# Optimization experiments

Hardware: AMD Instinct MI355X
Metric: run time of the kernel (lower is better)

## Reference

```python
import jax, jax.numpy as jnp
import numpy as np

HID, NH_FULL, K, GAMMA = 768, 12, 9, 2
HD = HID // NH_FULL            # 64
NH = NH_FULL // GAMMA          # 6
RH = HD * NH                   # 384 reduced hidden dim
OUT_HALF = HID // 2            # 384
B, S = 8, 1024


def setup_inputs() -> dict:
    key0 = jax.random.key(0)
    ks = jax.random.split(key0, 20)
    r = lambda i, shape, sc=0.02: (jax.random.normal(ks[i], shape, dtype=jnp.float32) * sc)
    inp = {
        'query': jax.random.normal(ks[0], (B, S, HID), dtype=jnp.float32),
        'mask': jnp.ones((B, 1, 1, S), dtype=jnp.int32),
        # q/k/v projections: hidden -> reduced
        'Wq': r(1, (HID, RH)), 'bq': jnp.zeros((RH,), jnp.float32),
        'Wk': r(2, (HID, RH)), 'bk': jnp.zeros((RH,), jnp.float32),
        'Wv': r(3, (HID, RH)), 'bv': jnp.zeros((RH,), jnp.float32),
        # depthwise separable conv: depthwise [HID,1,K] + pointwise [RH,HID]
        'dw_w': r(4, (HID, 1, K), 0.1), 'dw_b': jnp.zeros((HID,), jnp.float32),
        'pw_w': r(5, (RH, HID)), 'pw_b': jnp.zeros((RH,), jnp.float32),
        # self-attn output proj: reduced -> hidden//2
        'Wsa': r(6, (RH, OUT_HALF)), 'bsa': jnp.zeros((OUT_HALF,), jnp.float32),
        # dynamic kernel layer: reduced -> K*NH
        'Wdk': r(7, (RH, K * NH)), 'bdk': jnp.zeros((K * NH,), jnp.float32),
        # dynamic attn output proj: reduced -> hidden//2
        'Wda': r(8, (RH, OUT_HALF)), 'bda': jnp.zeros((OUT_HALF,), jnp.float32),
    }
    # self_attn=True requires query==key==value
    inp['key'] = inp['query']
    inp['value'] = inp['query']
    return inp


def _forward(query, key, value, mask, Wq, bq, Wk, bk, Wv, bv,
             dw_w, dw_b, pw_w, pw_b, Wsa, bsa, Wdk, bdk, Wda, bda):
    b, s, _ = query.shape
    q = query @ Wq + bq          # [B,S,RH]
    k = key @ Wk + bk
    v = value @ Wv + bv

    # ---- depthwise separable conv over key (seq axis), 'same' padding ----
    key_t = jnp.transpose(key, (0, 2, 1))  # [B,HID,S]
    dw = jax.lax.conv_general_dilated(
        key_t, dw_w, window_strides=(1,), padding=[(K // 2, K // 2)],
        feature_group_count=HID, dimension_numbers=('NCH', 'OIH', 'NCH'))
    dw = dw + dw_b[None, :, None]          # [B,HID,S]
    ks_feat = jnp.einsum('bhs,rh->bsr', dw, pw_w) + pw_b  # [B,S,RH]

    # ---- standard multi-head self-attention branch ----
    def split(x):  # [B,S,RH] -> [B,NH,S,HD]
        return x.reshape(b, s, NH, HD).transpose(0, 2, 1, 3)
    qh, kh, vh = split(q), split(k), split(v)
    scores = jnp.einsum('bhqd,bhkd->bhqk', qh, kh) / jnp.sqrt(jnp.float32(HD))
    scores = jnp.where(mask == 0, jnp.float32(-jnp.inf), scores)
    attn_wts = jax.nn.softmax(scores, axis=-1)             # [B,NH,S,S]
    attn_out = jnp.einsum('bhqk,bhkd->bhqd', attn_wts, vh)
    attn_out = attn_out.transpose(0, 2, 1, 3).reshape(b, s, RH)
    self_out = attn_out @ Wsa + bsa                         # [B,S,HID//2]

    # ---- span dynamic conv attention branch ----
    # unfold v into sliding windows: expanded[b,s,h,d,k] = v_pad[b, s+k, h*HD+d]
    v_pad = jnp.pad(v, ((0, 0), (K // 2, K // 2), (0, 0)))  # [B,S+K-1,RH]
    windows = jnp.stack([v_pad[:, i:i + s] for i in range(K)], axis=-1)  # [B,S,RH,K]
    windows = windows.reshape(b, s, NH, HD, K)
    dyn_logits = (q * ks_feat) @ Wdk + bdk                  # [B,S,K*NH]
    dyn_kernel = jax.nn.softmax(dyn_logits.reshape(b, s, NH, K), axis=-1)
    dyn_out = jnp.einsum('bshdk,bshk->bshd', windows, dyn_kernel).reshape(b, s, RH)
    dyn_out = dyn_out @ Wda + bda                           # [B,S,HID//2]

    return attn_wts, jnp.concatenate([self_out, dyn_out], axis=-1)


def reference(query, key, value, mask, Wq, bq, Wk, bk, Wv, bv,
              dw_w, dw_b, pw_w, pw_b, Wsa, bsa, Wdk, bdk, Wda, bda):
    return _forward(query, key, value, mask, Wq, bq, Wk, bk, Wv, bv,
                    dw_w, dw_b, pw_w, pw_b, Wsa, bsa, Wdk, bdk, Wda, bda)
```

## Files before the change

kernel.cpp:

```cpp
#include <hip/hip_runtime.h>
#include <math.h>

#define B 8
#define S 1024
#define HID 768
#define RH 384
#define NH 6
#define HD 64
#define KW 9
#define KNH 54
#define OUTHALF 384
#define QLD 1152
#define EXPSCALE 0.18033688f

typedef __attribute__((ext_vector_type(8))) short short8;
typedef __attribute__((ext_vector_type(4))) float f32x4;

#define SWZ(r, c) (((r) << 6) + ((c) ^ (((r) & 7) << 3)))

__device__ __forceinline__ ushort f2bf(float x) {
    unsigned u = __float_as_uint(x);
    u += 0x7FFF + ((u >> 16) & 1);
    return (ushort)(u >> 16);
}
__device__ __forceinline__ float bf2f(ushort u) {
    return __uint_as_float(((unsigned)u) << 16);
}
__device__ __forceinline__ short8 cvt8(const float* p) {
    short8 r;
    #pragma unroll
    for (int i = 0; i < 8; i++) r[i] = (short)f2bf(p[i]);
    return r;
}

__global__ __launch_bounds__(256) void cvt_dw_fused(
    const float* __restrict__ query, const float* __restrict__ dw_w,
    const float* __restrict__ dw_b, ushort* __restrict__ Xbf,
    ushort* __restrict__ dwout)
{
    int idx = blockIdx.x*256 + threadIdx.x;
    if (idx >= B*S*(HID/8)) return;
    int c0 = (idx % (HID/8))*8;
    int s  = (idx / (HID/8)) % S;
    int b  = idx / ((HID/8)*S);

    float ctr[8];
    *(float4*)&ctr[0] = *(const float4*)(query + ((size_t)b*S + s)*HID + c0);
    *(float4*)&ctr[4] = *(const float4*)(query + ((size_t)b*S + s)*HID + c0 + 4);
    *(short8*)(Xbf + ((size_t)b*S + s)*HID + c0) = cvt8(ctr);

    float acc[8];
    *(float4*)&acc[0] = *(const float4*)(dw_b + c0);
    *(float4*)&acc[4] = *(const float4*)(dw_b + c0 + 4);
    #pragma unroll
    for (int kk = 0; kk < KW; kk++) {
        int sp = s + kk - KW/2;
        if (sp >= 0 && sp < S) {
            float row[8];
            *(float4*)&row[0] = *(const float4*)(query + ((size_t)b*S + sp)*HID + c0);
            *(float4*)&row[4] = *(const float4*)(query + ((size_t)b*S + sp)*HID + c0 + 4);
            #pragma unroll
            for (int j = 0; j < 8; j++)
                acc[j] += row[j] * dw_w[(c0+j)*KW + kk];
        }
    }
    *(short8*)(dwout + ((size_t)b*S + s)*HID + c0) = cvt8(acc);
}

__global__ __launch_bounds__(256) void prep_weights(
    const float* __restrict__ Wq, const float* __restrict__ Wk, const float* __restrict__ Wv,
    const float* __restrict__ bq, const float* __restrict__ bk, const float* __restrict__ bv,
    const float* __restrict__ pw_w, const float* __restrict__ Wsa,
    const float* __restrict__ Wda, const float* __restrict__ Wdk,
    ushort* __restrict__ WqkvT, ushort* __restrict__ pw_bf,
    ushort* __restrict__ WsaT, ushort* __restrict__ WdaT, ushort* __restrict__ WdkT,
    float* __restrict__ bqkv)
{
    int i = blockIdx.x*256 + threadIdx.x;
    if (i < 884736) {
        int n = i / 768, kk = i % 768;
        int w = n / 384, nn = n % 384;
        const float* W = (w == 0) ? Wq : (w == 1) ? Wk : Wv;
        WqkvT[i] = f2bf(W[kk*384 + nn]);
        return;
    }
    i -= 884736;
    if (i < 294912) { pw_bf[i] = f2bf(pw_w[i]); return; }
    i -= 294912;
    if (i < 147456) {
        int n = i / 384, kk = i % 384;
        WsaT[i] = f2bf(Wsa[kk*384 + n]);
        return;
    }
    i -= 147456;
    if (i < 147456) {
        int n = i / 384, kk = i % 384;
        WdaT[i] = f2bf(Wda[kk*384 + n]);
        return;
    }
    i -= 147456;
    if (i < 49152) {
        int n = i / 384, kk = i % 384;
        WdkT[i] = (n < KNH) ? f2bf(Wdk[kk*KNH + n]) : (ushort)0;
        return;
    }
    i -= 49152;
    if (i < 1152) {
        bqkv[i] = (i < 384) ? bq[i] : (i < 768) ? bk[i-384] : bv[i-768];
    }
}

template<bool OUTBF>
__global__ __launch_bounds__(256) void gemm_mfma(
    const ushort* __restrict__ A, const ushort* __restrict__ Bt,
    const float* __restrict__ bias, void* __restrict__ Cout,
    int N, int Kd, int ldc)
{
    __shared__ __attribute__((aligned(16))) ushort As[128*32];
    __shared__ __attribute__((aligned(16))) ushort Bs[128*32];
    const int t = threadIdx.x;
    const int wave = t >> 6, lane = t & 63;
    const int lr = lane & 15, lg = lane >> 4;
    const int wr = wave >> 1, wc = wave & 1;
    const int bm = blockIdx.y * 128, bn = blockIdx.x * 128;

    f32x4 acc[4][4] = {};
    const int srow = t >> 1, sseg = t & 1;
    const ushort* Arow = A + (size_t)(bm + srow)*Kd + sseg*16;
    const ushort* Brow = Bt + (size_t)(bn + srow)*Kd + sseg*16;
    const int g0 = (sseg*2) ^ (srow & 3), g1 = (sseg*2 + 1) ^ (srow & 3);
    const int swz = lg ^ (lr & 3);

    for (int k0 = 0; k0 < Kd; k0 += 32) {
        short8 av0 = *(const short8*)(Arow + k0);
        short8 av1 = *(const short8*)(Arow + k0 + 8);
        short8 bv0 = *(const short8*)(Brow + k0);
        short8 bv1 = *(const short8*)(Brow + k0 + 8);
        __syncthreads();
        *(short8*)&As[srow*32 + g0*8] = av0;
        *(short8*)&As[srow*32 + g1*8] = av1;
        *(short8*)&Bs[srow*32 + g0*8] = bv0;
        *(short8*)&Bs[srow*32 + g1*8] = bv1;
        __syncthreads();
        short8 af[4], bfr[4];
        #pragma unroll
        for (int m = 0; m < 4; m++)
            af[m] = *(const short8*)&As[(wr*64 + m*16 + lr)*32 + swz*8];
        #pragma unroll
        for (int n = 0; n < 4; n++)
            bfr[n] = *(const short8*)&Bs[(wc*64 + n*16 + lr)*32 + swz*8];
        #pragma unroll
        for (int m = 0; m < 4; m++)
            #pragma unroll
            for (int n = 0; n < 4; n++)
                acc[m][n] = __builtin_amdgcn_mfma_f32_16x16x32_bf16(af[m], bfr[n], acc[m][n], 0, 0, 0);
    }

    #pragma unroll
    for (int m = 0; m < 4; m++) {
        #pragma unroll
        for (int n = 0; n < 4; n++) {
            int gcol = bn + wc*64 + n*16 + lr;
            if (gcol >= N) continue;
            float bz = bias[gcol];
            #pragma unroll
            for (int r = 0; r < 4; r++) {
                size_t grow = bm + wr*64 + m*16 + lg*4 + r;
                float val = acc[m][n][r] + bz;
                if (OUTBF) ((ushort*)Cout)[grow*ldc + gcol] = f2bf(val);
                else       ((float*)Cout)[grow*ldc + gcol] = val;
            }
        }
    }
}

template<bool OUTBF, bool DUAL>
__global__ __launch_bounds__(256) void gemm64(
    const ushort* __restrict__ A0, const ushort* __restrict__ Bt0,
    const float* __restrict__ bias0, void* __restrict__ C0,
    const ushort* __restrict__ A1, const ushort* __restrict__ Bt1,
    const float* __restrict__ bias1,
    int N, int Kd, int ldc)
{
    __shared__ __attribute__((aligned(16))) ushort As[64*32];
    __shared__ __attribute__((aligned(16))) ushort Bs[64*32];
    const ushort* A  = (DUAL && blockIdx.z) ? A1 : A0;
    const ushort* Bt = (DUAL && blockIdx.z) ? Bt1 : Bt0;
    const float* bias = (DUAL && blockIdx.z) ? bias1 : bias0;
    const int coff = (DUAL && blockIdx.z) ? OUTHALF : 0;

    const int t = threadIdx.x;
    const int wave = t >> 6, lane = t & 63;
    const int lr = lane & 15, lg = lane >> 4;
    const int wr = wave >> 1, wc = wave & 1;
    const int bm = blockIdx.y * 64, bn = blockIdx.x * 64;

    f32x4 acc[2][2] = {};
    const int srow = t >> 2, sseg = t & 3;
    const ushort* Arow = A + (size_t)(bm + srow)*Kd + sseg*8;
    const ushort* Brow = Bt + (size_t)(bn + srow)*Kd + sseg*8;
    const int gs = sseg ^ (srow & 3);
    const int swz = lg ^ (lr & 3);

    for (int k0 = 0; k0 < Kd; k0 += 32) {
        short8 av = *(const short8*)(Arow + k0);
        short8 bv = *(const short8*)(Brow + k0);
        __syncthreads();
        *(short8*)&As[srow*32 + gs*8] = av;
        *(short8*)&Bs[srow*32 + gs*8] = bv;
        __syncthreads();
        short8 af[2], bfr[2];
        #pragma unroll
        for (int m = 0; m < 2; m++)
            af[m] = *(const short8*)&As[(wr*32 + m*16 + lr)*32 + swz*8];
        #pragma unroll
        for (int n = 0; n < 2; n++)
            bfr[n] = *(const short8*)&Bs[(wc*32 + n*16 + lr)*32 + swz*8];
        #pragma unroll
        for (int m = 0; m < 2; m++)
            #pragma unroll
            for (int n = 0; n < 2; n++)
                acc[m][n] = __builtin_amdgcn_mfma_f32_16x16x32_bf16(af[m], bfr[n], acc[m][n], 0, 0, 0);
    }

    #pragma unroll
    for (int m = 0; m < 2; m++) {
        #pragma unroll
        for (int n = 0; n < 2; n++) {
            int gcol = bn + wc*32 + n*16 + lr;
            if (gcol >= N) continue;
            float bz = bias[gcol];
            #pragma unroll
            for (int r = 0; r < 4; r++) {
                size_t grow = bm + wr*32 + m*16 + lg*4 + r;
                float val = acc[m][n][r] + bz;
                if (OUTBF) ((ushort*)C0)[grow*ldc + gcol + coff] = f2bf(val);
                else       ((float*)C0)[grow*ldc + gcol + coff] = val;
            }
        }
    }
}

__global__ __launch_bounds__(64) void gemm_qksdk(
    const ushort* __restrict__ qkv, const float* __restrict__ ksf,
    const ushort* __restrict__ WdkT, const float* __restrict__ bdk,
    float* __restrict__ dynlog)
{
    const int lane = threadIdx.x;
    const int lr = lane & 15, lg = lane >> 4;
    const int r0 = blockIdx.x * 16;
    const int row = r0 + lr;

    f32x4 acc[4] = {};
    for (int ks = 0; ks < RH/32; ks++) {
        int k0 = ks*32 + lg*8;
        short8 qv = *(const short8*)(qkv + (size_t)row*QLD + k0);
        float kf[8];
        *(float4*)&kf[0] = *(const float4*)(ksf + (size_t)row*RH + k0);
        *(float4*)&kf[4] = *(const float4*)(ksf + (size_t)row*RH + k0 + 4);
        short8 afr;
        #pragma unroll
        for (int j = 0; j < 8; j++)
            afr[j] = (short)f2bf(bf2f((ushort)qv[j]) * kf[j]);
        #pragma unroll
        for (int t4 = 0; t4 < 4; t4++) {
            short8 bfr = *(const short8*)(WdkT + (size_t)(t4*16 + lr)*RH + k0);
            acc[t4] = __builtin_amdgcn_mfma_f32_16x16x32_bf16(afr, bfr, acc[t4], 0, 0, 0);
        }
    }
    #pragma unroll
    for (int t4 = 0; t4 < 4; t4++) {
        int n = t4*16 + lr;
        if (n >= KNH) continue;
        float bz = bdk[n];
        #pragma unroll
        for (int r = 0; r < 4; r++)
            dynlog[(size_t)(r0 + lg*4 + r)*KNH + n] = acc[t4][r] + bz;
    }
}

__global__ __launch_bounds__(256) void attn_fused(
    const ushort* __restrict__ qkv, const int* __restrict__ mask,
    float* __restrict__ out0, ushort* __restrict__ attnws)
{
    __shared__ __attribute__((aligned(16))) ushort Ks[64*64];
    __shared__ __attribute__((aligned(16))) ushort Vt[64*64];
    __shared__ __attribute__((aligned(16))) ushort Ps[4][16*64];

    const int b = blockIdx.z, h = blockIdx.y, q0 = blockIdx.x * 64;
    const int t = threadIdx.x;
    const int wave = t >> 6, lane = t & 63;
    const int lr = lane & 15, lg = lane >> 4;

    const ushort* qrow = qkv + (size_t)(b*S + q0 + wave*16 + lr)*QLD + h*HD;
    short8 aQ0 = *(const short8*)(qrow + lg*8);
    short8 aQ1 = *(const short8*)(qrow + 32 + lg*8);

    const int srow = t >> 2;
    const int sseg = t & 3;
    const int* mrow = mask + b*S;
    const ushort* kbase = qkv + RH;
    const ushort* vbase = qkv + 2*RH;

    float lsum[4] = {0.f, 0.f, 0.f, 0.f};

    for (int kc = 0; kc < S; kc += 64) {
        const ushort* kr = kbase + (size_t)(b*S + kc + srow)*QLD + h*HD + sseg*16;
        short8 kv0 = *(const short8*)(kr);
        short8 kv1 = *(const short8*)(kr + 8);
        __syncthreads();
        *(short8*)&Ks[SWZ(srow, sseg*16)]     = kv0;
        *(short8*)&Ks[SWZ(srow, sseg*16 + 8)] = kv1;
        __syncthreads();
        #pragma unroll
        for (int t4 = 0; t4 < 4; t4++) {
            short8 b0 = *(const short8*)&Ks[SWZ(t4*16 + lr, lg*8)];
            short8 b1 = *(const short8*)&Ks[SWZ(t4*16 + lr, 32 + lg*8)];
            f32x4 c = {0.f, 0.f, 0.f, 0.f};
            c = __builtin_amdgcn_mfma_f32_16x16x32_bf16(aQ0, b0, c, 0, 0, 0);
            c = __builtin_amdgcn_mfma_f32_16x16x32_bf16(aQ1, b1, c, 0, 0, 0);
            float add = mrow[kc + t4*16 + lr] ? 0.f : -1e30f;
            #pragma unroll
            for (int r = 0; r < 4; r++)
                lsum[r] += exp2f(c[r]*EXPSCALE + add);
        }
    }
    #pragma unroll
    for (int r = 0; r < 4; r++) {
        #pragma unroll
        for (int off = 1; off < 16; off <<= 1)
            lsum[r] += __shfl_xor(lsum[r], off, 16);
    }
    float inv[4];
    #pragma unroll
    for (int r = 0; r < 4; r++) inv[r] = 1.f / lsum[r];

    f32x4 o[4] = {};
    ushort* Psw = &Ps[wave][0];
    const size_t obase = ((size_t)((b*NH + h)*S) + q0 + wave*16) * (size_t)S;

    for (int kc = 0; kc < S; kc += 64) {
        const ushort* kr = kbase + (size_t)(b*S + kc + srow)*QLD + h*HD + sseg*16;
        short8 kv0 = *(const short8*)(kr);
        short8 kv1 = *(const short8*)(kr + 8);
        ushort vb[16];
        #pragma unroll
        for (int i = 0; i < 16; i++)
            vb[i] = vbase[(size_t)(b*S + kc + sseg*16 + i)*QLD + h*HD + srow];
        __syncthreads();
        *(short8*)&Ks[SWZ(srow, sseg*16)]     = kv0;
        *(short8*)&Ks[SWZ(srow, sseg*16 + 8)] = kv1;
        *(short8*)&Vt[SWZ(srow, sseg*16)]     = *(short8*)&vb[0];
        *(short8*)&Vt[SWZ(srow, sseg*16 + 8)] = *(short8*)&vb[8];
        __syncthreads();

        #pragma unroll
        for (int t4 = 0; t4 < 4; t4++) {
            short8 b0 = *(const short8*)&Ks[SWZ(t4*16 + lr, lg*8)];
            short8 b1 = *(const short8*)&Ks[SWZ(t4*16 + lr, 32 + lg*8)];
            f32x4 c = {0.f, 0.f, 0.f, 0.f};
            c = __builtin_amdgcn_mfma_f32_16x16x32_bf16(aQ0, b0, c, 0, 0, 0);
            c = __builtin_amdgcn_mfma_f32_16x16x32_bf16(aQ1, b1, c, 0, 0, 0);
            float add = mrow[kc + t4*16 + lr] ? 0.f : -1e30f;
            #pragma unroll
            for (int r = 0; r < 4; r++) {
                float p = exp2f(c[r]*EXPSCALE + add) * inv[r];
                out0[obase + (size_t)(lg*4 + r)*S + kc + t4*16 + lr] = p;
                Psw[SWZ(lg*4 + r, t4*16 + lr)] = f2bf(p);
            }
        }
        #pragma unroll
        for (int kh = 0; kh < 2; kh++) {
            short8 pa = *(const short8*)&Psw[SWZ(lr, kh*32 + lg*8)];
            #pragma unroll
            for (int dt = 0; dt < 4; dt++) {
                short8 vv = *(const short8*)&Vt[SWZ(dt*16 + lr, kh*32 + lg*8)];
                o[dt] = __builtin_amdgcn_mfma_f32_16x16x32_bf16(pa, vv, o[dt], 0, 0, 0);
            }
        }
    }

    #pragma unroll
    for (int dt = 0; dt < 4; dt++)
        #pragma unroll
        for (int r = 0; r < 4; r++)
            attnws[(size_t)(b*S + q0 + wave*16 + lg*4 + r)*RH + h*HD + dt*16 + lr] = f2bf(o[dt][r]);
}

__global__ __launch_bounds__(256) void dyn_conv(
    const float* __restrict__ logits, const ushort* __restrict__ qkv,
    ushort* __restrict__ dynout)
{
    int idx = blockIdx.x*256 + threadIdx.x;
    if (idx >= B*S*(RH/4)) return;
    int r4 = (idx % (RH/4))*4;
    int s  = (idx / (RH/4)) % S;
    int b  = idx / ((RH/4)*S);
    int h  = r4 / HD;
    const float* lg = logits + ((size_t)b*S + s)*KNH + h*KW;
    float mx = lg[0];
    #pragma unroll
    for (int kk = 1; kk < KW; kk++) mx = fmaxf(mx, lg[kk]);
    float e[KW], sum = 0.f;
    #pragma unroll
    for (int kk = 0; kk < KW; kk++) { e[kk] = __expf(lg[kk]-mx); sum += e[kk]; }
    float inv = 1.f/sum;
    float acc[4] = {0.f, 0.f, 0.f, 0.f};
    const ushort* vbase = qkv + 2*RH;
    #pragma unroll
    for (int kk = 0; kk < KW; kk++) {
        int sp = s + kk - KW/2;
        if (sp >= 0 && sp < S) {
            const ushort* vp = vbase + (size_t)(b*S + sp)*QLD + r4;
            #pragma unroll
            for (int j = 0; j < 4; j++) acc[j] += bf2f(vp[j]) * e[kk];
        }
    }
    ushort4 o;
    o.x = f2bf(acc[0]*inv); o.y = f2bf(acc[1]*inv);
    o.z = f2bf(acc[2]*inv); o.w = f2bf(acc[3]*inv);
    *(ushort4*)(dynout + ((size_t)b*S + s)*RH + r4) = o;
}

extern "C" void kernel_launch(void* const* d_in, const int* in_sizes, int n_in,
                              void* d_out, int out_size, void* d_ws, size_t ws_size,
                              hipStream_t stream) {
    const float* query = (const float*)d_in[0];
    const int*   mask  = (const int*)d_in[1];
    const float* Wq    = (const float*)d_in[2];
    const float* bq    = (const float*)d_in[3];
    const float* Wk    = (const float*)d_in[4];
    const float* bk    = (const float*)d_in[5];
    const float* Wv    = (const float*)d_in[6];
    const float* bv    = (const float*)d_in[7];
    const float* dw_w  = (const float*)d_in[8];
    const float* dw_b  = (const float*)d_in[9];
    const float* pw_w  = (const float*)d_in[10];
    const float* pw_b  = (const float*)d_in[11];
    const float* Wsa   = (const float*)d_in[12];
    const float* bsa   = (const float*)d_in[13];
    const float* Wdk   = (const float*)d_in[14];
    const float* bdk   = (const float*)d_in[15];
    const float* Wda   = (const float*)d_in[16];
    const float* bda   = (const float*)d_in[17];

    float* out0 = (float*)d_out;
    float* out1 = out0 + (size_t)B*NH*S*S;

    char* wsb = (char*)d_ws;
    size_t off = 0;
    auto alloc = [&](size_t bytes) { char* p = wsb + off; off += (bytes + 255) & ~255ull; return p; };
    ushort* Xbf    = (ushort*)alloc((size_t)B*S*HID*2);
    ushort* qkvbf  = (ushort*)alloc((size_t)B*S*QLD*2);
    ushort* dwbf   = (ushort*)alloc((size_t)B*S*HID*2);
    float*  ksf    = (float*) alloc((size_t)B*S*RH*4);
    ushort* attnbf = (ushort*)alloc((size_t)B*S*RH*2);
    ushort* dynbf  = (ushort*)alloc((size_t)B*S*RH*2);
    float*  dynlog = (float*) alloc((size_t)B*S*KNH*4);
    ushort* WqkvT  = (ushort*)alloc((size_t)QLD*HID*2);
    ushort* pw_bf  = (ushort*)alloc((size_t)RH*HID*2);
    ushort* WsaT   = (ushort*)alloc((size_t)RH*RH*2);
    ushort* WdaT   = (ushort*)alloc((size_t)RH*RH*2);
    ushort* WdkT   = (ushort*)alloc((size_t)128*RH*2);
    float*  bqkv   = (float*) alloc((size_t)QLD*4);

    const int M = B*S;

    prep_weights<<<(1524864 + 255)/256, 256, 0, stream>>>(
        Wq, Wk, Wv, bq, bk, bv, pw_w, Wsa, Wda, Wdk,
        WqkvT, pw_bf, WsaT, WdaT, WdkT, bqkv);

    cvt_dw_fused<<<(M*(HID/8) + 255)/256, 256, 0, stream>>>(query, dw_w, dw_b, Xbf, dwbf);

    gemm_mfma<true><<<dim3(QLD/128, M/128), 256, 0, stream>>>(
        Xbf, WqkvT, bqkv, qkvbf, QLD, HID, QLD);

    gemm64<false, false><<<dim3(RH/64, M/64), 256, 0, stream>>>(
        dwbf, pw_bf, pw_b, ksf, nullptr, nullptr, nullptr, RH, HID, RH);

    attn_fused<<<dim3(S/64, NH, B), 256, 0, stream>>>(qkvbf, mask, out0, attnbf);

    gemm_qksdk<<<M/16, 64, 0, stream>>>(qkvbf, ksf, WdkT, bdk, dynlog);

    dyn_conv<<<(M*(RH/4) + 255)/256, 256, 0, stream>>>(dynlog, qkvbf, dynbf);

    gemm64<false, true><<<dim3(OUTHALF/64, M/64, 2), 256, 0, stream>>>(
        attnbf, WsaT, bsa, out1, dynbf, WdaT, bda, OUTHALF, RH, HID);
}
```

Before: 310.9 us.

## Prefetch next tiles in GEMMs and attention, store ksf as bf16, nontemporal stores

Register-level software prefetching is added to both GEMM kernels and both attention passes, so the global loads for the next K/V or A/B tile are issued after the LDS store barrier and overlap with the MFMA compute on the current tile. The depthwise-pointwise intermediate ksf is now written and read as bf16 instead of fp32, halving its traffic. The large attention-weights output uses nontemporal stores to avoid polluting cache. These add register pressure and slightly reduce precision of the ks features.

```diff
diff --git a/kernel.cpp b/kernel.cpp
--- a/kernel.cpp
+++ b/kernel.cpp
@@ -131,17 +131,24 @@
     const int g0 = (sseg*2) ^ (srow & 3), g1 = (sseg*2 + 1) ^ (srow & 3);
     const int swz = lg ^ (lr & 3);
 
+    short8 av0 = *(const short8*)(Arow);
+    short8 av1 = *(const short8*)(Arow + 8);
+    short8 bv0 = *(const short8*)(Brow);
+    short8 bv1 = *(const short8*)(Brow + 8);
+
     for (int k0 = 0; k0 < Kd; k0 += 32) {
-        short8 av0 = *(const short8*)(Arow + k0);
-        short8 av1 = *(const short8*)(Arow + k0 + 8);
-        short8 bv0 = *(const short8*)(Brow + k0);
-        short8 bv1 = *(const short8*)(Brow + k0 + 8);
         __syncthreads();
         *(short8*)&As[srow*32 + g0*8] = av0;
         *(short8*)&As[srow*32 + g1*8] = av1;
         *(short8*)&Bs[srow*32 + g0*8] = bv0;
         *(short8*)&Bs[srow*32 + g1*8] = bv1;
         __syncthreads();
+        if (k0 + 32 < Kd) {
+            av0 = *(const short8*)(Arow + k0 + 32);
+            av1 = *(const short8*)(Arow + k0 + 40);
+            bv0 = *(const short8*)(Brow + k0 + 32);
+            bv1 = *(const short8*)(Brow + k0 + 40);
+        }
         short8 af[4], bfr[4];
         #pragma unroll
         for (int m = 0; m < 4; m++)
@@ -202,13 +209,18 @@
     const int gs = sseg ^ (srow & 3);
     const int swz = lg ^ (lr & 3);
 
+    short8 av = *(const short8*)(Arow);
+    short8 bv = *(const short8*)(Brow);
+
     for (int k0 = 0; k0 < Kd; k0 += 32) {
-        short8 av = *(const short8*)(Arow + k0);
-        short8 bv = *(const short8*)(Brow + k0);
         __syncthreads();
         *(short8*)&As[srow*32 + gs*8] = av;
         *(short8*)&Bs[srow*32 + gs*8] = bv;
         __syncthreads();
+        if (k0 + 32 < Kd) {
+            av = *(const short8*)(Arow + k0 + 32);
+            bv = *(const short8*)(Brow + k0 + 32);
+        }
         short8 af[2], bfr[2];
         #pragma unroll
         for (int m = 0; m < 2; m++)
@@ -242,7 +254,7 @@
 }
 
 __global__ __launch_bounds__(64) void gemm_qksdk(
-    const ushort* __restrict__ qkv, const float* __restrict__ ksf,
+    const ushort* __restrict__ qkv, const ushort* __restrict__ ksf,
     const ushort* __restrict__ WdkT, const float* __restrict__ bdk,
     float* __restrict__ dynlog)
 {
@@ -255,13 +267,11 @@
     for (int ks = 0; ks < RH/32; ks++) {
         int k0 = ks*32 + lg*8;
         short8 qv = *(const short8*)(qkv + (size_t)row*QLD + k0);
-        float kf[8];
-        *(float4*)&kf[0] = *(const float4*)(ksf + (size_t)row*RH + k0);
-        *(float4*)&kf[4] = *(const float4*)(ksf + (size_t)row*RH + k0 + 4);
+        short8 kv = *(const short8*)(ksf + (size_t)row*RH + k0);
         short8 afr;
         #pragma unroll
         for (int j = 0; j < 8; j++)
-            afr[j] = (short)f2bf(bf2f((ushort)qv[j]) * kf[j]);
+            afr[j] = (short)f2bf(bf2f((ushort)qv[j]) * bf2f((ushort)kv[j]));
         #pragma unroll
         for (int t4 = 0; t4 < 4; t4++) {
             short8 bfr = *(const short8*)(WdkT + (size_t)(t4*16 + lr)*RH + k0);
@@ -299,19 +309,23 @@
     const int srow = t >> 2;
     const int sseg = t & 3;
     const int* mrow = mask + b*S;
-    const ushort* kbase = qkv + RH;
-    const ushort* vbase = qkv + 2*RH;
+    const ushort* krbase = qkv + RH + (size_t)(b*S + srow)*QLD + h*HD + sseg*16;
+    const ushort* vbase  = qkv + 2*RH + (size_t)b*S*QLD + h*HD + srow;
 
     float lsum[4] = {0.f, 0.f, 0.f, 0.f};
 
+    short8 kv0 = *(const short8*)(krbase);
+    short8 kv1 = *(const short8*)(krbase + 8);
     for (int kc = 0; kc < S; kc += 64) {
-        const ushort* kr = kbase + (size_t)(b*S + kc + srow)*QLD + h*HD + sseg*16;
-        short8 kv0 = *(const short8*)(kr);
-        short8 kv1 = *(const short8*)(kr + 8);
         __syncthreads();
         *(short8*)&Ks[SWZ(srow, sseg*16)]     = kv0;
         *(short8*)&Ks[SWZ(srow, sseg*16 + 8)] = kv1;
         __syncthreads();
+        if (kc + 64 < S) {
+            const ushort* kr = krbase + (size_t)(kc + 64)*QLD;
+            kv0 = *(const short8*)(kr);
+            kv1 = *(const short8*)(kr + 8);
+        }
         #pragma unroll
         for (int t4 = 0; t4 < 4; t4++) {
             short8 b0 = *(const short8*)&Ks[SWZ(t4*16 + lr, lg*8)];
@@ -339,20 +353,29 @@
     ushort* Psw = &Ps[wave][0];
     const size_t obase = ((size_t)((b*NH + h)*S) + q0 + wave*16) * (size_t)S;
 
+    kv0 = *(const short8*)(krbase);
+    kv1 = *(const short8*)(krbase + 8);
+    ushort vb[16];
+    #pragma unroll
+    for (int i = 0; i < 16; i++)
+        vb[i] = vbase[(size_t)(sseg*16 + i)*QLD];
+
     for (int kc = 0; kc < S; kc += 64) {
-        const ushort* kr = kbase + (size_t)(b*S + kc + srow)*QLD + h*HD + sseg*16;
-        short8 kv0 = *(const short8*)(kr);
-        short8 kv1 = *(const short8*)(kr + 8);
-        ushort vb[16];
-        #pragma unroll
-        for (int i = 0; i < 16; i++)
-            vb[i] = vbase[(size_t)(b*S + kc + sseg*16 + i)*QLD + h*HD + srow];
         __syncthreads();
         *(short8*)&Ks[SWZ(srow, sseg*16)]     = kv0;
         *(short8*)&Ks[SWZ(srow, sseg*16 + 8)] = kv1;
         *(short8*)&Vt[SWZ(srow, sseg*16)]     = *(short8*)&vb[0];
         *(short8*)&Vt[SWZ(srow, sseg*16 + 8)] = *(short8*)&vb[8];
         __syncthreads();
+        if (kc + 64 < S) {
+            const ushort* kr = krbase + (size_t)(kc + 64)*QLD;
+            kv0 = *(const short8*)(kr);
+            kv1 = *(const short8*)(kr + 8);
+            const ushort* vp = vbase + (size_t)(kc + 64)*QLD;
+            #pragma unroll
+            for (int i = 0; i < 16; i++)
+                vb[i] = vp[(size_t)(sseg*16 + i)*QLD];
+        }
 
         #pragma unroll
         for (int t4 = 0; t4 < 4; t4++) {
@@ -365,7 +388,7 @@
             #pragma unroll
             for (int r = 0; r < 4; r++) {
                 float p = exp2f(c[r]*EXPSCALE + add) * inv[r];
-                out0[obase + (size_t)(lg*4 + r)*S + kc + t4*16 + lr] = p;
+                __builtin_nontemporal_store(p, &out0[obase + (size_t)(lg*4 + r)*S + kc + t4*16 + lr]);
                 Psw[SWZ(lg*4 + r, t4*16 + lr)] = f2bf(p);
             }
         }
@@ -453,7 +476,7 @@
     ushort* Xbf    = (ushort*)alloc((size_t)B*S*HID*2);
     ushort* qkvbf  = (ushort*)alloc((size_t)B*S*QLD*2);
     ushort* dwbf   = (ushort*)alloc((size_t)B*S*HID*2);
-    float*  ksf    = (float*) alloc((size_t)B*S*RH*4);
+    ushort* ksf    = (ushort*)alloc((size_t)B*S*RH*2);
     ushort* attnbf = (ushort*)alloc((size_t)B*S*RH*2);
     ushort* dynbf  = (ushort*)alloc((size_t)B*S*RH*2);
     float*  dynlog = (float*) alloc((size_t)B*S*KNH*4);
@@ -475,7 +498,7 @@
     gemm_mfma<true><<<dim3(QLD/128, M/128), 256, 0, stream>>>(
         Xbf, WqkvT, bqkv, qkvbf, QLD, HID, QLD);
 
-    gemm64<false, false><<<dim3(RH/64, M/64), 256, 0, stream>>>(
+    gemm64<true, false><<<dim3(RH/64, M/64), 256, 0, stream>>>(
         dwbf, pw_bf, pw_b, ksf, nullptr, nullptr, nullptr, RH, HID, RH);
 
     attn_fused<<<dim3(S/64, NH, B), 256, 0, stream>>>(qkvbf, mask, out0, attnbf);
```

After: 303.5 us. 1.02x faster.
